# Kernel optimization log

Measured on AMD Instinct MI355X. Metric: run time of the kernel, lower is better.

## Reference

```python
import jax, jax.numpy as jnp
import numpy as np

D_MODEL = 768
BATCH = 4096
RANK_DIST = [(4, 512), (8, 256), (16, 128), (32, 64), (64, 32)]


@jax.custom_vjp
def jumprelu(x):
    # hard threshold at 0 in fwd; full straight-through estimator in bwd
    return x * (x > 0.0).astype(x.dtype)


def _jr_fwd(x):
    return jumprelu(x), None


def _jr_bwd(res, g):
    return (g,)


jumprelu.defvjp(_jr_fwd, _jr_bwd)


def setup_inputs() -> dict:
    key = jax.random.key(0)
    keys = jax.random.split(key, 1 + 3 * len(RANK_DIST))
    inp = {"x": jax.random.normal(keys[0], (BATCH, D_MODEL), dtype=jnp.float32)}
    for i, (n, r) in enumerate(RANK_DIST):
        kV, kU, kE = keys[1 + 3 * i], keys[2 + 3 * i], keys[3 + 3 * i]
        scale = (1.0 / (D_MODEL * r)) ** 0.25
        inp[f"V{i}"] = scale * jax.random.normal(kV, (n, r, D_MODEL), dtype=jnp.float32)
        inp[f"U{i}"] = scale * jax.random.normal(kU, (n, D_MODEL, r), dtype=jnp.float32)
        enc = jax.random.normal(kE, (n, D_MODEL), dtype=jnp.float32)
        inp[f"enc{i}"] = enc / jnp.linalg.norm(enc, axis=1, keepdims=True)
        inp[f"b{i}"] = jnp.full((n,), -1.0, dtype=jnp.float32)
    return inp


def _group_forward(x, V, U, enc, b):
    n, r, d = V.shape
    pre = x @ enc.T - b                      # (b, n)
    gate = jumprelu(pre)                     # (b, n)
    Vx = jnp.einsum("nrd,bd->nbr", V, x)    # (n, b, r)
    # fused: UVx gated by gate then summed over transforms n
    out = jnp.einsum("ndr,nbr,bn->bd", U, Vx, gate)  # (b, d)
    u_norms = jnp.linalg.norm(U.reshape(n, -1), axis=1)
    v_norms = jnp.linalg.norm(V.reshape(n, -1), axis=1)
    frob = u_norms * v_norms / jnp.sqrt(jnp.asarray(d * r, dtype=x.dtype))
    return out, gate, frob


def reference(x, V0, U0, enc0, b0, V1, U1, enc1, b1, V2, U2, enc2, b2,
              V3, U3, enc3, b3, V4, U4, enc4, b4):
    Vs = [V0, V1, V2, V3, V4]
    Us = [U0, U1, U2, U3, U4]
    encs = [enc0, enc1, enc2, enc3, enc4]
    bs = [b0, b1, b2, b3, b4]
    output = jnp.zeros_like(x)
    total_sparsity = jnp.asarray(0.0, dtype=x.dtype)
    total_active = jnp.asarray(0.0, dtype=x.dtype)
    gate_acts = []
    for V, U, enc, b in zip(Vs, Us, encs, bs):
        g_out, gate, frob = _group_forward(x, V, U, enc, b)
        output = output + g_out
        mean_abs_gate = jnp.abs(gate).mean(axis=0)
        total_sparsity = total_sparsity + (jnp.tanh(mean_abs_gate) * frob).sum()
        total_active = total_active + (gate > 0).astype(x.dtype).sum(axis=1).mean()
        gate_acts.append(gate)
    return (output, total_sparsity, total_active, *gate_acts)
```

## Files before the change

kernel.cpp:

```cpp
#include <hip/hip_runtime.h>

#define BATCH 4096
#define DM 768
#define LTOT 10240
#define NG 124

typedef __bf16 bf16x8 __attribute__((ext_vector_type(8)));
typedef short short8 __attribute__((ext_vector_type(8)));
typedef float f32x4 __attribute__((ext_vector_type(4)));

struct Ptr5 { const float* p[5]; };

__device__ __forceinline__ unsigned short f2bf(float f) {
    unsigned u = __builtin_bit_cast(unsigned, f);
    unsigned r = (u + 0x7FFFu + ((u >> 16) & 1u)) >> 16;
    return (unsigned short)r;
}


__global__ __launch_bounds__(256) void prep_k(const float* __restrict__ x,
                                              Ptr5 vp, Ptr5 up, Ptr5 ep, Ptr5 bp,
                                              unsigned short* __restrict__ vb,
                                              unsigned short* __restrict__ w2t,
                                              unsigned short* __restrict__ xb,
                                              unsigned short* __restrict__ encb,
                                              float* __restrict__ b_all,
                                              float* __restrict__ vn2,
                                              float* __restrict__ un2) {
    const int basen[5] = {0, 4, 12, 28, 60};
    int bx = blockIdx.x;
    int tid = threadIdx.x;
    if (bx < 1920) {
        __shared__ float swave[4];
        int isV = bx < 960;
        int wb = isV ? bx : bx - 960;
        int g = wb / 192;
        int within = wb - g * 192;
        int bpseg = 48 >> g;
        int nloc = within / bpseg;
        const float* src = isV ? vp.p[g] : up.p[g];
        int r = 512 >> g, lr = 9 - g;
        float ss = 0.f;
        #pragma unroll
        for (int i = 0; i < 8; i++) {
            int j = within * 2048 + i * 256 + tid;
            float4 v = ((const float4*)src)[j];
            ss += v.x*v.x + v.y*v.y + v.z*v.z + v.w*v.w;
            ushort4 o;
            o.x = f2bf(v.x); o.y = f2bf(v.y); o.z = f2bf(v.z); o.w = f2bf(v.w);
            if (isV) {
                ((ushort4*)vb)[(size_t)(g * 192 + within) * 2048 + i * 256 + tid] = o;
            } else {
                int idx = j * 4;
                int rr = idx & (r - 1);
                int t2 = idx >> lr;
                int d  = t2 % DM;
                int n  = t2 / DM;
                size_t dst = (size_t)d * LTOT + (size_t)(g << 11) + (size_t)n * r + rr;
                *(ushort4*)(w2t + dst) = o;
            }
        }
        #pragma unroll
        for (int off = 32; off > 0; off >>= 1) ss += __shfl_down(ss, off);
        if ((tid & 63) == 0) swave[tid >> 6] = ss;
        __syncthreads();
        if (tid == 0) {
            float t = (swave[0] + swave[1]) + (swave[2] + swave[3]);
            float* dstN = isV ? vn2 : un2;
            atomicAdd(&dstN[basen[g] + nloc], t);
        }
    } else if (bx < 2304) {
        int base = (bx - 1920) * 2048;
        #pragma unroll
        for (int i = 0; i < 8; i++) {
            int j = base + i * 256 + tid;
            float4 v = ((const float4*)x)[j];
            ushort4 o;
            o.x = f2bf(v.x); o.y = f2bf(v.y); o.z = f2bf(v.z); o.w = f2bf(v.w);
            ((ushort4*)xb)[j] = o;
        }
    } else if (bx < 2397) {
        int j = (bx - 2304) * 256 + tid;
        int n = j / 192, c = j - n * 192;
        int g = (n < 4) ? 0 : (n < 12) ? 1 : (n < 28) ? 2 : (n < 60) ? 3 : 4;
        int ni = n - basen[g];
        float4 v = ((const float4*)ep.p[g])[ni * 192 + c];
        ushort4 o;
        o.x = f2bf(v.x); o.y = f2bf(v.y); o.z = f2bf(v.z); o.w = f2bf(v.w);
        ((ushort4*)encb)[n * 192 + c] = o;
    } else {
        if (tid < NG) {
            int n = tid;
            int g = (n < 4) ? 0 : (n < 12) ? 1 : (n < 28) ? 2 : (n < 60) ? 3 : 4;
            b_all[n] = bp.p[g][n - basen[g]];
        }
    }
}


__global__ __launch_bounds__(256) void gatestats_k(const float* __restrict__ gate_ws,
                                                   float* __restrict__ gate_sum,
                                                   float* __restrict__ active) {
    __shared__ float s0[124], s1[124];
    __shared__ unsigned cntsh;
    int tid = threadIdx.x;
    if (tid == 0) cntsh = 0u;
    int b0 = blockIdx.x * 32;
    unsigned cl = 0;
    float s = 0.f;
    if (tid < 248) {
        int n = (tid < 124) ? tid : tid - 124;
        int rp = (tid < 124) ? 0 : 1;
        for (int r = rp; r < 32; r += 2) {
            float v = gate_ws[(size_t)(b0 + r) * NG + n];
            s += v;
            cl += (v > 0.f) ? 1u : 0u;
        }
        if (rp) s1[n] = s; else s0[n] = s;
    }
    if (cl) atomicAdd(&cntsh, cl);
    __syncthreads();
    if (tid < 124) {
        float t = s0[tid] + s1[tid];
        if (t != 0.f) atomicAdd(&gate_sum[tid], t);
    }
    if (tid == 0 && cntsh) atomicAdd(active, (float)cntsh);
}

template <int ROWS, int NT>
__device__ __forceinline__ void stage(const unsigned short* __restrict__ src, int ld,
                                      unsigned short* lds, int wv, int lane) {
    int rsub = lane >> 3;
    int colb = ((lane ^ rsub) & 7) * 8;
    #pragma unroll
    for (int i = 0; i < ROWS * 8 / NT; i++) {
        int c = i * (NT / 64) + wv;
        const unsigned short* gp = src + (size_t)(c * 8 + rsub) * ld + colb;
        __builtin_amdgcn_global_load_lds((const __attribute__((address_space(1))) void*)gp,
                                         (__attribute__((address_space(3))) void*)(lds + c * 512),
                                         16, 0, 0);
    }
}

template <int BM, int BN, int EPI, int NT>
__global__ __launch_bounds__(NT) void gemm_nt(const unsigned short* __restrict__ A,
                                              const unsigned short* __restrict__ Bm,
                                              int Kblk, int lda, int ldb,
                                              void* __restrict__ Cout,
                                              const float* __restrict__ gate, int ldc,
                                              float* __restrict__ extra) {
    __shared__ unsigned short lA[BM * 64];
    __shared__ unsigned short lB[BN * 64];
    int tid = threadIdx.x, wave = tid >> 6, lane = tid & 63;
    constexpr int WN = BN / 64;
    int wm = wave / WN, wn = wave % WN;
    int m0 = blockIdx.x * BM, n0 = blockIdx.y * BN;
    A  += (size_t)m0 * lda + (size_t)blockIdx.z * Kblk;
    Bm += (size_t)n0 * ldb + (size_t)blockIdx.z * Kblk;
    f32x4 acc[4][4] = {};
    int lan15 = lane & 15, quad = lane >> 4;
    int sw = lan15 & 7;

    for (int k0 = 0; k0 < Kblk; k0 += 64) {
        stage<BM, NT>(A + k0, lda, lA, wave, lane);
        stage<BN, NT>(Bm + k0, ldb, lB, wave, lane);
        __syncthreads();
        #pragma unroll
        for (int kk = 0; kk < 2; kk++) {
            int kb = kk * 4 + quad;
            int kel = (kb ^ sw) * 8;
            bf16x8 af[4], bfr[4];
            #pragma unroll
            for (int t = 0; t < 4; t++) {
                short8 ra = *(const short8*)(lA + (size_t)(wm * 64 + t * 16 + lan15) * 64 + kel);
                short8 rb = *(const short8*)(lB + (size_t)(wn * 64 + t * 16 + lan15) * 64 + kel);
                af[t]  = __builtin_bit_cast(bf16x8, ra);
                bfr[t] = __builtin_bit_cast(bf16x8, rb);
            }
            #pragma unroll
            for (int mt = 0; mt < 4; mt++)
                #pragma unroll
                for (int nt = 0; nt < 4; nt++)
                    acc[mt][nt] = __builtin_amdgcn_mfma_f32_16x16x32_bf16(af[mt], bfr[nt],
                                                                          acc[mt][nt], 0, 0, 0);
        }
        __syncthreads();
    }

    const int basen[5] = {0, 4, 12, 28, 60};
    if (EPI == 0) {
        unsigned short* H = (unsigned short*)Cout;
        #pragma unroll
        for (int mt = 0; mt < 4; mt++) {
            __syncthreads();
            #pragma unroll
            for (int nt = 0; nt < 4; nt++) {
                int col = n0 + wn * 64 + nt * 16 + lan15;
                int g = col >> 11;
                int ngl = basen[g] + ((col & 2047) >> (9 - g));
                #pragma unroll
                for (int rg = 0; rg < 4; rg++) {
                    int grow = m0 + wm * 64 + mt * 16 + quad * 4 + rg;
                    float gv = gate[(size_t)grow * NG + ngl];
                    lA[wave * 1024 + (quad * 4 + rg) * 64 + nt * 16 + lan15] =
                        f2bf(acc[mt][nt][rg] * gv);
                }
            }
            __syncthreads();
            #pragma unroll
            for (int i = 0; i < 2; i++) {
                int f = i * NT + tid;
                int R = f >> 5;
                int u = f & 31;
                int wv2 = ((R >> 4) << 2) + (u >> 3);
                short8 vread = *(const short8*)(lA + wv2 * 1024 + (R & 15) * 64 + (u & 7) * 8);
                int grow = m0 + (R >> 4) * 64 + mt * 16 + (R & 15);
                *(short8*)(H + (size_t)grow * ldc + n0 + u * 8) = vread;
            }
        }
    } else if (EPI == 1) {
        float* P = (float*)Cout;
        P += (size_t)blockIdx.z * gridDim.x * BM * ldc;
        #pragma unroll
        for (int nt = 0; nt < 4; nt++) {
            int col = n0 + wn * 64 + nt * 16 + lan15;
            #pragma unroll
            for (int mt = 0; mt < 4; mt++) {
                int r0 = m0 + wm * 64 + mt * 16 + quad * 4;
                #pragma unroll
                for (int rg = 0; rg < 4; rg++)
                    P[(size_t)(r0 + rg) * ldc + col] = acc[mt][nt][rg];
            }
        }
    } else {
        float* GW = (float*)Cout;
        float* OG = extra;
        const size_t baseg[5] = {3145730ull, 3145730ull + 16384, 3145730ull + 49152,
                                 3145730ull + 114688, 3145730ull + 245760};
        #pragma unroll
        for (int nt = 0; nt < 4; nt++) {
            int col = wn * 64 + nt * 16 + lan15;
            if (col < NG) {
                int g = (col < 4) ? 0 : (col < 12) ? 1 : (col < 28) ? 2 : (col < 60) ? 3 : 4;
                int ni = col - basen[g];
                int w = 4 << g;
                float bv = gate[col];
                #pragma unroll
                for (int mt = 0; mt < 4; mt++) {
                    int r0 = m0 + wm * 64 + mt * 16 + quad * 4;
                    #pragma unroll
                    for (int rg = 0; rg < 4; rg++) {
                        float pre = acc[mt][nt][rg] - bv;
                        float gt = pre > 0.f ? pre : 0.f;
                        GW[(size_t)(r0 + rg) * ldc + col] = gt;
                        OG[baseg[g] + (size_t)(r0 + rg) * w + ni] = gt;
                    }
                }
            }
        }
    }
}


__global__ __launch_bounds__(256) void reduce_k(const float4* __restrict__ P,
                                                float4* __restrict__ out, int quarter,
                                                const float* __restrict__ st,
                                                float* __restrict__ o2) {
    int i = blockIdx.x * 256 + threadIdx.x;
    float4 a = P[i], b = P[i + quarter], c = P[i + 2 * quarter], d = P[i + 3 * quarter];
    float4 o;
    o.x = (a.x + b.x) + (c.x + d.x);
    o.y = (a.y + b.y) + (c.y + d.y);
    o.z = (a.z + b.z) + (c.z + d.z);
    o.w = (a.w + b.w) + (c.w + d.w);
    out[i] = o;
    if (blockIdx.x == 0) {
        __shared__ float sh[128];
        int t = threadIdx.x;
        if (t < 128) {
            float v = 0.f;
            if (t < NG) {
                int g = (t < 4) ? 0 : (t < 12) ? 1 : (t < 28) ? 2 : (t < 60) ? 3 : 4;
                float rr = (float)(512 >> g);
                float mean = st[t] * (1.0f / BATCH);
                float frob = sqrtf(st[124 + t] * st[248 + t]) / sqrtf(768.0f * rr);
                v = tanhf(mean) * frob;
            }
            sh[t] = v;
        }
        __syncthreads();
        for (int s = 64; s > 0; s >>= 1) {
            if (threadIdx.x < s) sh[threadIdx.x] += sh[threadIdx.x + s];
            __syncthreads();
        }
        if (threadIdx.x == 0) { o2[0] = sh[0]; o2[1] = st[372] * (1.0f / BATCH); }
    }
}


extern "C" void kernel_launch(void* const* d_in, const int* in_sizes, int n_in,
                              void* d_out, int out_size, void* d_ws, size_t ws_size,
                              hipStream_t stream) {
    const float* x = (const float*)d_in[0];
    Ptr5 vp, up, ep, bp;
    for (int g = 0; g < 5; g++) {
        vp.p[g] = (const float*)d_in[1 + 4 * g];
        up.p[g] = (const float*)d_in[2 + 4 * g];
        ep.p[g] = (const float*)d_in[3 + 4 * g];
        bp.p[g] = (const float*)d_in[4 + 4 * g];
    }
    float* out = (float*)d_out;
    char* ws = (char*)d_ws;
    size_t off = 0;
    unsigned short* xb   = (unsigned short*)(ws + off); off += (size_t)BATCH * DM * 2;
    unsigned short* vb   = (unsigned short*)(ws + off); off += (size_t)LTOT * DM * 2;
    unsigned short* w2t  = (unsigned short*)(ws + off); off += (size_t)LTOT * DM * 2;
    unsigned short* encb = (unsigned short*)(ws + off); off += (size_t)128 * DM * 2;
    float* b_all         = (float*)(ws + off);          off += 512;
    float* gate_ws       = (float*)(ws + off);          off += (size_t)BATCH * NG * 4;
    float* stats         = (float*)(ws + off);          off += 4096;
    size_t fixed = off;
    int CB = BATCH;
    while (CB > 128 && fixed + (size_t)CB * LTOT * 2 + 4ull * CB * DM * 4 > ws_size) CB >>= 1;
    unsigned short* Hg  = (unsigned short*)(ws + fixed);
    float* partial      = (float*)(ws + fixed + (size_t)CB * LTOT * 2);

    hipMemsetAsync(stats, 0, 4096, stream);

    prep_k<<<dim3(2398), 256, 0, stream>>>(
        x, vp, up, ep, bp, vb, w2t, xb, encb, b_all, stats + 248, stats + 124);
    gemm_nt<128, 128, 2, 256><<<dim3(BATCH / 128, 1, 1), 256, 0, stream>>>(
        xb, encb, DM, DM, DM, (void*)gate_ws, b_all, NG, out);
    gatestats_k<<<dim3(BATCH / 32), 256, 0, stream>>>(gate_ws, stats, stats + 372);

    int nch = BATCH / CB;
    for (int c = 0; c < nch; c++) {
        gemm_nt<128, 256, 0, 512><<<dim3(CB / 128, LTOT / 256, 1), 512, 0, stream>>>(
            xb + (size_t)c * CB * DM, vb, DM, DM, DM,
            (void*)Hg, gate_ws + (size_t)c * CB * NG, LTOT, nullptr);
        gemm_nt<128, 128, 1, 256><<<dim3(CB / 128, DM / 128, 4), 256, 0, stream>>>(
            Hg, w2t, LTOT / 4, LTOT, LTOT,
            (void*)partial, nullptr, DM, nullptr);
        reduce_k<<<dim3(CB * 192 / 256), 256, 0, stream>>>(
            (const float4*)partial, (float4*)(out + (size_t)c * CB * DM), CB * DM / 4,
            stats, out + (size_t)BATCH * DM);
    }
}
```

Measured before the change: 337.9 us.

## Fuse gate GEMM and gate statistics into prep kernel, drop memset and atomics

The encoder gate GEMM now runs as 32 extra blocks inside the prep kernel. They read fp32 x and enc directly, convert to bf16 while staging into LDS, and compute the gate, per-column sums and the active count in the epilogue. This removes three launches (the memset, the separate gate GEMM and the gatestats kernel) plus the encb/b_all staging. Global atomics are replaced with per-block slots that reduce_k sums at the end. The cost is a slower, non-async staging path for the gate GEMM, and its blocks now share the prep launch with the conversion blocks.

```diff
diff --git a/kernel.cpp b/kernel.cpp
--- a/kernel.cpp
+++ b/kernel.cpp
@@ -15,6 +15,13 @@
     unsigned u = __builtin_bit_cast(unsigned, f);
     unsigned r = (u + 0x7FFFu + ((u >> 16) & 1u)) >> 16;
     return (unsigned short)r;
+}
+
+__device__ __forceinline__ short8 pack8(float4 a, float4 b) {
+    union { unsigned short u[8]; short8 s; } o;
+    o.u[0] = f2bf(a.x); o.u[1] = f2bf(a.y); o.u[2] = f2bf(a.z); o.u[3] = f2bf(a.w);
+    o.u[4] = f2bf(b.x); o.u[5] = f2bf(b.y); o.u[6] = f2bf(b.z); o.u[7] = f2bf(b.w);
+    return o.s;
 }
 
 
@@ -23,21 +30,117 @@
                                               unsigned short* __restrict__ vb,
                                               unsigned short* __restrict__ w2t,
                                               unsigned short* __restrict__ xb,
-                                              unsigned short* __restrict__ encb,
-                                              float* __restrict__ b_all,
-                                              float* __restrict__ vn2,
-                                              float* __restrict__ un2) {
+                                              float* __restrict__ gate_ws,
+                                              float* __restrict__ outg,
+                                              float* __restrict__ vslot,
+                                              float* __restrict__ uslot,
+                                              float* __restrict__ gslot,
+                                              float* __restrict__ aslot) {
     const int basen[5] = {0, 4, 12, 28, 60};
     int bx = blockIdx.x;
     int tid = threadIdx.x;
-    if (bx < 1920) {
+    if (bx < 32) {
+        __shared__ unsigned short lA[128 * 64];
+        __shared__ unsigned short lB[128 * 64];
+        __shared__ float sgs[128];
+        __shared__ float sac;
+        int wave = tid >> 6, lane = tid & 63;
+        int wm = wave >> 1, wn = wave & 1;
+        int lan15 = lane & 15, quad = lane >> 4;
+        int sw = lan15 & 7;
+        int m0 = bx * 128;
+        f32x4 acc[4][4] = {};
+        for (int k0 = 0; k0 < DM; k0 += 64) {
+            __syncthreads();
+            #pragma unroll
+            for (int i = 0; i < 4; i++) {
+                int gidx = i * 256 + tid;
+                int row = gidx >> 3, kb = gidx & 7;
+                int r7 = row & 7;
+                int la = (row >> 3) * 512 + r7 * 64 + (kb ^ r7) * 8;
+                int sidx = (m0 + row) * 192 + (k0 >> 2) + kb * 2;
+                float4 a0 = ((const float4*)x)[sidx];
+                float4 a1 = ((const float4*)x)[sidx + 1];
+                *(short8*)(lA + la) = pack8(a0, a1);
+                float4 b0 = {0.f, 0.f, 0.f, 0.f}, b1 = {0.f, 0.f, 0.f, 0.f};
+                if (row < NG) {
+                    int g = (row < 4) ? 0 : (row < 12) ? 1 : (row < 28) ? 2 :
+                            (row < 60) ? 3 : 4;
+                    int ni = row - basen[g];
+                    int eidx = ni * 192 + (k0 >> 2) + kb * 2;
+                    b0 = ((const float4*)ep.p[g])[eidx];
+                    b1 = ((const float4*)ep.p[g])[eidx + 1];
+                }
+                *(short8*)(lB + la) = pack8(b0, b1);
+            }
+            __syncthreads();
+            #pragma unroll
+            for (int kk = 0; kk < 2; kk++) {
+                int kb = kk * 4 + quad;
+                int kel = (kb ^ sw) * 8;
+                bf16x8 af[4], bfr[4];
+                #pragma unroll
+                for (int t = 0; t < 4; t++) {
+                    short8 ra = *(const short8*)(lA + (wm * 64 + t * 16 + lan15) * 64 + kel);
+                    short8 rb = *(const short8*)(lB + (wn * 64 + t * 16 + lan15) * 64 + kel);
+                    af[t]  = __builtin_bit_cast(bf16x8, ra);
+                    bfr[t] = __builtin_bit_cast(bf16x8, rb);
+                }
+                #pragma unroll
+                for (int mt = 0; mt < 4; mt++)
+                    #pragma unroll
+                    for (int nt = 0; nt < 4; nt++)
+                        acc[mt][nt] = __builtin_amdgcn_mfma_f32_16x16x32_bf16(
+                            af[mt], bfr[nt], acc[mt][nt], 0, 0, 0);
+            }
+        }
+        if (tid < 128) sgs[tid] = 0.f;
+        if (tid == 0) sac = 0.f;
+        __syncthreads();
+        const size_t baseg[5] = {3145730ull, 3145730ull + 16384, 3145730ull + 49152,
+                                 3145730ull + 114688, 3145730ull + 245760};
+        float cnt = 0.f;
+        #pragma unroll
+        for (int nt = 0; nt < 4; nt++) {
+            int col = wn * 64 + nt * 16 + lan15;
+            float cs = 0.f;
+            if (col < NG) {
+                int g = (col < 4) ? 0 : (col < 12) ? 1 : (col < 28) ? 2 :
+                        (col < 60) ? 3 : 4;
+                int ni = col - basen[g];
+                int w = 4 << g;
+                float bv = bp.p[g][ni];
+                #pragma unroll
+                for (int mt = 0; mt < 4; mt++) {
+                    int r0 = m0 + wm * 64 + mt * 16 + quad * 4;
+                    #pragma unroll
+                    for (int rg = 0; rg < 4; rg++) {
+                        float pre = acc[mt][nt][rg] - bv;
+                        float gt = pre > 0.f ? pre : 0.f;
+                        gate_ws[(size_t)(r0 + rg) * NG + col] = gt;
+                        outg[baseg[g] + (size_t)(r0 + rg) * w + ni] = gt;
+                        cs += gt;
+                        if (pre > 0.f) cnt += 1.f;
+                    }
+                }
+                cs += __shfl_xor(cs, 16);
+                cs += __shfl_xor(cs, 32);
+                if (quad == 0) atomicAdd(&sgs[col], cs);
+            }
+        }
+        #pragma unroll
+        for (int off = 32; off > 0; off >>= 1) cnt += __shfl_xor(cnt, off);
+        if (lane == 0) atomicAdd(&sac, cnt);
+        __syncthreads();
+        if (tid < NG) gslot[bx * NG + tid] = sgs[tid];
+        if (tid == 0) aslot[bx] = sac;
+    } else if (bx < 1952) {
         __shared__ float swave[4];
-        int isV = bx < 960;
-        int wb = isV ? bx : bx - 960;
+        int cb = bx - 32;
+        int isV = cb < 960;
+        int wb = isV ? cb : cb - 960;
         int g = wb / 192;
         int within = wb - g * 192;
-        int bpseg = 48 >> g;
-        int nloc = within / bpseg;
         const float* src = isV ? vp.p[g] : up.p[g];
         int r = 512 >> g, lr = 9 - g;
         float ss = 0.f;
@@ -66,11 +169,10 @@
         __syncthreads();
         if (tid == 0) {
             float t = (swave[0] + swave[1]) + (swave[2] + swave[3]);
-            float* dstN = isV ? vn2 : un2;
-            atomicAdd(&dstN[basen[g] + nloc], t);
-        }
-    } else if (bx < 2304) {
-        int base = (bx - 1920) * 2048;
+            (isV ? vslot : uslot)[wb] = t;
+        }
+    } else {
+        int base = (bx - 1952) * 2048;
         #pragma unroll
         for (int i = 0; i < 8; i++) {
             int j = base + i * 256 + tid;
@@ -79,52 +181,7 @@
             o.x = f2bf(v.x); o.y = f2bf(v.y); o.z = f2bf(v.z); o.w = f2bf(v.w);
             ((ushort4*)xb)[j] = o;
         }
-    } else if (bx < 2397) {
-        int j = (bx - 2304) * 256 + tid;
-        int n = j / 192, c = j - n * 192;
-        int g = (n < 4) ? 0 : (n < 12) ? 1 : (n < 28) ? 2 : (n < 60) ? 3 : 4;
-        int ni = n - basen[g];
-        float4 v = ((const float4*)ep.p[g])[ni * 192 + c];
-        ushort4 o;
-        o.x = f2bf(v.x); o.y = f2bf(v.y); o.z = f2bf(v.z); o.w = f2bf(v.w);
-        ((ushort4*)encb)[n * 192 + c] = o;
-    } else {
-        if (tid < NG) {
-            int n = tid;
-            int g = (n < 4) ? 0 : (n < 12) ? 1 : (n < 28) ? 2 : (n < 60) ? 3 : 4;
-            b_all[n] = bp.p[g][n - basen[g]];
-        }
-    }
-}
-
-
-__global__ __launch_bounds__(256) void gatestats_k(const float* __restrict__ gate_ws,
-                                                   float* __restrict__ gate_sum,
-                                                   float* __restrict__ active) {
-    __shared__ float s0[124], s1[124];
-    __shared__ unsigned cntsh;
-    int tid = threadIdx.x;
-    if (tid == 0) cntsh = 0u;
-    int b0 = blockIdx.x * 32;
-    unsigned cl = 0;
-    float s = 0.f;
-    if (tid < 248) {
-        int n = (tid < 124) ? tid : tid - 124;
-        int rp = (tid < 124) ? 0 : 1;
-        for (int r = rp; r < 32; r += 2) {
-            float v = gate_ws[(size_t)(b0 + r) * NG + n];
-            s += v;
-            cl += (v > 0.f) ? 1u : 0u;
-        }
-        if (rp) s1[n] = s; else s0[n] = s;
-    }
-    if (cl) atomicAdd(&cntsh, cl);
-    __syncthreads();
-    if (tid < 124) {
-        float t = s0[tid] + s1[tid];
-        if (t != 0.f) atomicAdd(&gate_sum[tid], t);
-    }
-    if (tid == 0 && cntsh) atomicAdd(active, (float)cntsh);
+    }
 }
 
 template <int ROWS, int NT>
@@ -147,8 +204,7 @@
                                               const unsigned short* __restrict__ Bm,
                                               int Kblk, int lda, int ldb,
                                               void* __restrict__ Cout,
-                                              const float* __restrict__ gate, int ldc,
-                                              float* __restrict__ extra) {
+                                              const float* __restrict__ gate, int ldc) {
     __shared__ unsigned short lA[BM * 64];
     __shared__ unsigned short lB[BN * 64];
     int tid = threadIdx.x, wave = tid >> 6, lane = tid & 63;
@@ -218,7 +274,7 @@
                 *(short8*)(H + (size_t)grow * ldc + n0 + u * 8) = vread;
             }
         }
-    } else if (EPI == 1) {
+    } else {
         float* P = (float*)Cout;
         P += (size_t)blockIdx.z * gridDim.x * BM * ldc;
         #pragma unroll
@@ -232,39 +288,16 @@
                     P[(size_t)(r0 + rg) * ldc + col] = acc[mt][nt][rg];
             }
         }
-    } else {
-        float* GW = (float*)Cout;
-        float* OG = extra;
-        const size_t baseg[5] = {3145730ull, 3145730ull + 16384, 3145730ull + 49152,
-                                 3145730ull + 114688, 3145730ull + 245760};
-        #pragma unroll
-        for (int nt = 0; nt < 4; nt++) {
-            int col = wn * 64 + nt * 16 + lan15;
-            if (col < NG) {
-                int g = (col < 4) ? 0 : (col < 12) ? 1 : (col < 28) ? 2 : (col < 60) ? 3 : 4;
-                int ni = col - basen[g];
-                int w = 4 << g;
-                float bv = gate[col];
-                #pragma unroll
-                for (int mt = 0; mt < 4; mt++) {
-                    int r0 = m0 + wm * 64 + mt * 16 + quad * 4;
-                    #pragma unroll
-                    for (int rg = 0; rg < 4; rg++) {
-                        float pre = acc[mt][nt][rg] - bv;
-                        float gt = pre > 0.f ? pre : 0.f;
-                        GW[(size_t)(r0 + rg) * ldc + col] = gt;
-                        OG[baseg[g] + (size_t)(r0 + rg) * w + ni] = gt;
-                    }
-                }
-            }
-        }
     }
 }
 
 
 __global__ __launch_bounds__(256) void reduce_k(const float4* __restrict__ P,
                                                 float4* __restrict__ out, int quarter,
-                                                const float* __restrict__ st,
+                                                const float* __restrict__ vslot,
+                                                const float* __restrict__ uslot,
+                                                const float* __restrict__ gslot,
+                                                const float* __restrict__ aslot,
                                                 float* __restrict__ o2) {
     int i = blockIdx.x * 256 + threadIdx.x;
     float4 a = P[i], b = P[i + quarter], c = P[i + 2 * quarter], d = P[i + 3 * quarter];
@@ -276,24 +309,37 @@
     out[i] = o;
     if (blockIdx.x == 0) {
         __shared__ float sh[128];
+        const int basen[5] = {0, 4, 12, 28, 60};
         int t = threadIdx.x;
         if (t < 128) {
             float v = 0.f;
             if (t < NG) {
                 int g = (t < 4) ? 0 : (t < 12) ? 1 : (t < 28) ? 2 : (t < 60) ? 3 : 4;
+                int nloc = t - basen[g];
+                int bpseg = 48 >> g;
+                float vs = 0.f, us = 0.f;
+                int base = g * 192 + nloc * bpseg;
+                for (int j = 0; j < bpseg; j++) { vs += vslot[base + j]; us += uslot[base + j]; }
+                float gs = 0.f;
+                for (int bb = 0; bb < 32; bb++) gs += gslot[bb * NG + t];
                 float rr = (float)(512 >> g);
-                float mean = st[t] * (1.0f / BATCH);
-                float frob = sqrtf(st[124 + t] * st[248 + t]) / sqrtf(768.0f * rr);
+                float mean = gs * (1.0f / BATCH);
+                float frob = sqrtf(us * vs) / sqrtf(768.0f * rr);
                 v = tanhf(mean) * frob;
             }
             sh[t] = v;
+        }
+        if (t == 128) {
+            float asum = 0.f;
+            for (int bb = 0; bb < 32; bb++) asum += aslot[bb];
+            o2[1] = asum * (1.0f / BATCH);
         }
         __syncthreads();
         for (int s = 64; s > 0; s >>= 1) {
             if (threadIdx.x < s) sh[threadIdx.x] += sh[threadIdx.x + s];
             __syncthreads();
         }
-        if (threadIdx.x == 0) { o2[0] = sh[0]; o2[1] = st[372] * (1.0f / BATCH); }
+        if (threadIdx.x == 0) o2[0] = sh[0];
     }
 }
 
@@ -315,34 +361,31 @@
     unsigned short* xb   = (unsigned short*)(ws + off); off += (size_t)BATCH * DM * 2;
     unsigned short* vb   = (unsigned short*)(ws + off); off += (size_t)LTOT * DM * 2;
     unsigned short* w2t  = (unsigned short*)(ws + off); off += (size_t)LTOT * DM * 2;
-    unsigned short* encb = (unsigned short*)(ws + off); off += (size_t)128 * DM * 2;
-    float* b_all         = (float*)(ws + off);          off += 512;
     float* gate_ws       = (float*)(ws + off);          off += (size_t)BATCH * NG * 4;
-    float* stats         = (float*)(ws + off);          off += 4096;
+    float* vslot         = (float*)(ws + off);          off += 960 * 4;
+    float* uslot         = (float*)(ws + off);          off += 960 * 4;
+    float* gslot         = (float*)(ws + off);          off += 32 * NG * 4;
+    float* aslot         = (float*)(ws + off);          off += 32 * 4 + 256;
     size_t fixed = off;
     int CB = BATCH;
     while (CB > 128 && fixed + (size_t)CB * LTOT * 2 + 4ull * CB * DM * 4 > ws_size) CB >>= 1;
     unsigned short* Hg  = (unsigned short*)(ws + fixed);
     float* partial      = (float*)(ws + fixed + (size_t)CB * LTOT * 2);
 
-    hipMemsetAsync(stats, 0, 4096, stream);
-
-    prep_k<<<dim3(2398), 256, 0, stream>>>(
-        x, vp, up, ep, bp, vb, w2t, xb, encb, b_all, stats + 248, stats + 124);
-    gemm_nt<128, 128, 2, 256><<<dim3(BATCH / 128, 1, 1), 256, 0, stream>>>(
-        xb, encb, DM, DM, DM, (void*)gate_ws, b_all, NG, out);
-    gatestats_k<<<dim3(BATCH / 32), 256, 0, stream>>>(gate_ws, stats, stats + 372);
+    prep_k<<<dim3(2336), 256, 0, stream>>>(
+        x, vp, up, ep, bp, vb, w2t, xb, gate_ws, out,
+        vslot, uslot, gslot, aslot);
 
     int nch = BATCH / CB;
     for (int c = 0; c < nch; c++) {
         gemm_nt<128, 256, 0, 512><<<dim3(CB / 128, LTOT / 256, 1), 512, 0, stream>>>(
             xb + (size_t)c * CB * DM, vb, DM, DM, DM,
-            (void*)Hg, gate_ws + (size_t)c * CB * NG, LTOT, nullptr);
+            (void*)Hg, gate_ws + (size_t)c * CB * NG, LTOT);
         gemm_nt<128, 128, 1, 256><<<dim3(CB / 128, DM / 128, 4), 256, 0, stream>>>(
             Hg, w2t, LTOT / 4, LTOT, LTOT,
-            (void*)partial, nullptr, DM, nullptr);
+            (void*)partial, nullptr, DM);
         reduce_k<<<dim3(CB * 192 / 256), 256, 0, stream>>>(
             (const float4*)partial, (float4*)(out + (size_t)c * CB * DM), CB * DM / 4,
-            stats, out + (size_t)BATCH * DM);
-    }
-}
+            vslot, uslot, gslot, aslot, out + (size_t)BATCH * DM);
+    }
+}
```

Result: no change. 340.7 us (+0.8%).
